# Kernel optimization log

Hardware: AMD Instinct MI355X
Metric: run time of the kernel (lower is better)

The kernel has to match this reference:

```python
import jax, jax.numpy as jnp
import numpy as np

B, P = 8, 1000          # batch_size, num_prots
N = B * P               # total PPI nodes
E = 512000              # edges (avg degree 64)
F_HPO = 1024            # HPO feature dim (num_features)
F_MOLP = 8192           # protein molecular feature dim (hardcoded)
F_MOLD = 1024           # drug molecular feature dim (hardcoded)
D = 200
EPS = 1e-8              # torch CosineSimilarity default eps


def leaky(x):
    return jax.nn.leaky_relu(x, 0.2)


def gcn_improved(x, W, b, src, dst):
    # PyG GCNConv(improved=True): A_hat = A + 2*I, symmetrically normalized.
    h = x @ W                                                   # [N,200]
    deg = jnp.zeros((x.shape[0],), x.dtype).at[dst].add(1.0) + 2.0
    dinv = jax.lax.rsqrt(deg)
    norm = dinv[src] * dinv[dst]                                # [E]
    out = jnp.zeros_like(h).at[dst].add(norm[:, None] * h[src])  # gather->scale->scatter
    out = out + (2.0 * dinv * dinv)[:, None] * h                # self loops with weight 2
    return out + b


def setup_inputs() -> dict:
    key = jax.random.key(0)
    ks = jax.random.split(key, 30)
    def W(i, shape):
        return jax.random.normal(ks[i], shape, jnp.float32) * (1.0 / float(np.sqrt(shape[0])))
    def bvec(i, n):
        return jax.random.normal(ks[i], (n,), jnp.float32) * 0.01
    return {
        # forward inputs
        'PPI_x': jax.random.normal(ks[0], (N, F_HPO), jnp.float32),
        'protein_mol_feature': jax.random.normal(ks[1], (N, F_MOLP), jnp.float32),
        'drug_feature': jax.random.normal(ks[2], (B, F_HPO), jnp.float32),
        'drug_mol_feature': jax.random.normal(ks[3], (B, F_MOLD), jnp.float32),
        'edge_index': jax.random.randint(ks[4], (2, E), 0, N, dtype=jnp.int32),
        # frozen HPO model heads (assumed Linear -> 200)
        'hpo_drug_W': W(5, (F_HPO, D)), 'hpo_drug_b': bvec(6, D),
        'hpo_prot_W': W(7, (F_HPO, D)), 'hpo_prot_b': bvec(8, D),
        # mol_protein_model: 8192 -> 256 -> 200
        'mp_W1': W(9, (F_MOLP, 256)), 'mp_b1': bvec(10, 256),
        'mp_W2': W(11, (256, D)), 'mp_b2': bvec(12, D),
        # mol_drug_model: 1024 -> 256 -> 200
        'md_W1': W(13, (F_MOLD, 256)), 'md_b1': bvec(14, 256),
        'md_W2': W(15, (256, D)), 'md_b2': bvec(16, D),
        # fusion linears
        'pl1_W': W(17, (2 * D, D)), 'pl1_b': bvec(18, D),
        'dl1_W': W(19, (2 * D, D)), 'dl1_b': bvec(20, D),
        'dl2_W': W(21, (D, D)), 'dl2_b': bvec(22, D),
        # GCN layers
        'g1_W': W(23, (D, D)), 'g1_b': bvec(24, D),
        'g2_W': W(25, (D, D)), 'g2_b': bvec(26, D),
    }


def reference(PPI_x, protein_mol_feature, drug_feature, drug_mol_feature, edge_index,
              hpo_drug_W, hpo_drug_b, hpo_prot_W, hpo_prot_b,
              mp_W1, mp_b1, mp_W2, mp_b2, md_W1, md_b1, md_W2, md_b2,
              pl1_W, pl1_b, dl1_W, dl1_b, dl2_W, dl2_b,
              g1_W, g1_b, g2_W, g2_b):
    src, dst = edge_index[0], edge_index[1]
    # protein branch (dropout is identity in eval)
    px = PPI_x @ hpo_prot_W + hpo_prot_b                                 # [N,200]
    pm = leaky(protein_mol_feature @ mp_W1 + mp_b1) @ mp_W2 + mp_b2      # [N,200]
    px = leaky(jnp.concatenate([px, pm], axis=1))                        # [N,400]
    px = px @ pl1_W + pl1_b                                              # [N,200]
    # drug branch
    df = drug_feature @ hpo_drug_W + hpo_drug_b                          # [B,200]
    dm = leaky(drug_mol_feature @ md_W1 + md_b1) @ md_W2 + md_b2         # [B,200]
    d = leaky(jnp.concatenate([dm, df], axis=1))                         # [B,400]
    d = leaky(d @ dl1_W + dl1_b)                                         # [B,200]
    d = d @ dl2_W + dl2_b                                                # [B,200]
    d = jnp.repeat(d, P, axis=0)                                         # [B*P,200]
    # two stacked GCN layers (no nonlinearity between, as in source)
    px = gcn_improved(px, g1_W, g1_b, src, dst)
    px = gcn_improved(px, g2_W, g2_b, src, dst)
    # per-row cosine similarity (torch.nn.CosineSimilarity(dim=1))
    num = jnp.sum(d * px, axis=1)
    den = jnp.maximum(jnp.linalg.norm(d, axis=1), EPS) * jnp.maximum(jnp.linalg.norm(px, axis=1), EPS)
    sim = num / den
    return jax.nn.sigmoid(sim.reshape(B, P))
```

## Files before the change

kernel.cpp:

```cpp
#include <hip/hip_runtime.h>
#include <cstdint>
#include <cstddef>

typedef uint16_t u16;
typedef __bf16 bf16x8 __attribute__((ext_vector_type(8)));
typedef short  s16x8  __attribute__((ext_vector_type(8)));
typedef float  f32x4  __attribute__((ext_vector_type(4)));

__device__ __forceinline__ u16 f2b(float f) {
    union { float f; uint32_t u; } v; v.f = f;
    uint32_t u = v.u;
    uint32_t r = (u + 0x7FFFu + ((u >> 16) & 1u)) >> 16;
    return (u16)r;
}
__device__ __forceinline__ float b2f(u16 h) {
    union { uint32_t u; float f; } v; v.u = ((uint32_t)h) << 16;
    return v.f;
}
__device__ __forceinline__ float leakyf(float x) { return x > 0.f ? x : 0.2f * x; }
__device__ __forceinline__ void unp4(uint2 u, float& f0, float& f1, float& f2, float& f3) {
    union { uint32_t u; float f; } t;
    t.u = u.x << 16;          f0 = t.f;
    t.u = u.x & 0xffff0000u;  f1 = t.f;
    t.u = u.y << 16;          f2 = t.f;
    t.u = u.y & 0xffff0000u;  f3 = t.f;
}

static constexpr int NN = 8000;
static constexpr int EE = 512000;
static constexpr int BB = 8;

#define GLOAD_LDS16(gp, lp)                                                              \
    __builtin_amdgcn_global_load_lds((const __attribute__((address_space(1))) void*)(gp), \
                                     (__attribute__((address_space(3))) void*)(lp), 16, 0, 0)

__global__ void conv_wT(const float* __restrict__ W, int Wn, int rows, int rowOff,
                        u16* __restrict__ Bt, int Kpad, int kOff, int kSpan) {
    __shared__ u16 tile[64][65];
    const int kb = blockIdx.x * 64, nb = blockIdx.y * 64;
    const int tid = threadIdx.x;
    const int ln = tid & 63, lw = tid >> 6;
    #pragma unroll
    for (int r = 0; r < 16; r++) {
        int kk = kb + lw * 16 + r;
        int n  = nb + ln;
        float v = (kk < rows && n < Wn) ? W[(size_t)(rowOff + kk) * Wn + n] : 0.f;
        tile[ln][lw * 16 + r] = f2b(v);
    }
    __syncthreads();
    #pragma unroll
    for (int r = 0; r < 16; r++) {
        int nl = lw * 16 + r;
        int kk = kb + ln;
        if (kk < kSpan) Bt[(size_t)(nb + nl) * Kpad + kOff + kk] = tile[nl][ln];
    }
}

__global__ void conv_wT5(const float* W_mp2, const float* W_pl1, const float* W_g1, const float* W_g2,
                         u16* Btmp2, u16* Btpl1, u16* Btg1, u16* Btg2) {
    __shared__ u16 tile[64][65];
    const float* W; int Wn, rows, rowOff; u16* Bt; int Kpad, kOff, kSpan;
    switch (blockIdx.z) {
        case 0: W = W_mp2; Wn = 200; rows = 256; rowOff = 0;   Bt = Btmp2; Kpad = 256; kOff = 0;   kSpan = 256; break;
        case 1: W = W_pl1; Wn = 200; rows = 200; rowOff = 0;   Bt = Btpl1; Kpad = 512; kOff = 0;   kSpan = 256; break;
        case 2: W = W_pl1; Wn = 200; rows = 200; rowOff = 200; Bt = Btpl1; Kpad = 512; kOff = 256; kSpan = 256; break;
        case 3: W = W_g1;  Wn = 200; rows = 200; rowOff = 0;   Bt = Btg1;  Kpad = 256; kOff = 0;   kSpan = 256; break;
        default:W = W_g2;  Wn = 200; rows = 200; rowOff = 0;   Bt = Btg2;  Kpad = 256; kOff = 0;   kSpan = 256; break;
    }
    const int kb = blockIdx.x * 64, nb = blockIdx.y * 64;
    const int tid = threadIdx.x;
    const int ln = tid & 63, lw = tid >> 6;
    #pragma unroll
    for (int r = 0; r < 16; r++) {
        int kk = kb + lw * 16 + r;
        int n  = nb + ln;
        float v = (kk < rows && n < Wn) ? W[(size_t)(rowOff + kk) * Wn + n] : 0.f;
        tile[ln][lw * 16 + r] = f2b(v);
    }
    __syncthreads();
    #pragma unroll
    for (int r = 0; r < 16; r++) {
        int nl = lw * 16 + r;
        int kk = kb + ln;
        if (kk < kSpan) Bt[(size_t)(nb + nl) * Kpad + kOff + kk] = tile[nl][ln];
    }
}

__global__ void padvec5(const float* p0, int n0, float* d0,
                        const float* p1, int n1, float* d1,
                        const float* p2, int n2, float* d2,
                        const float* p3, int n3, float* d3,
                        const float* p4, int n4, float* d4) {
    const float* p; int n; float* d;
    switch (blockIdx.x) {
        case 0: p = p0; n = n0; d = d0; break;
        case 1: p = p1; n = n1; d = d1; break;
        case 2: p = p2; n = n2; d = d2; break;
        case 3: p = p3; n = n3; d = d3; break;
        default: p = p4; n = n4; d = d4; break;
    }
    int i = threadIdx.x;
    d[i] = (p != nullptr && i < n) ? p[i] : 0.f;
}

__global__ void zero_i32(int* __restrict__ p, int n) {
    int i = blockIdx.x * 256 + threadIdx.x;
    if (i < n) p[i] = 0;
}

template<int BM>
__global__ __launch_bounds__(256) void gemm_kernel(
    const void* __restrict__ Ap, int a_is_f32, int lda,
    const u16* __restrict__ Bt, int K, int kLen,
    const float* __restrict__ bias,
    void* __restrict__ Cp, int cmode, int ldc, int do_leaky, size_t partStride) {
    constexpr int MREP = BM / 16;
    __shared__ u16 As[BM][72];
    __shared__ u16 Bs[16384];
    const int tid  = threadIdx.x;
    const int m0   = blockIdx.x * BM;
    const int kStart = blockIdx.y * kLen;
    const int wave = tid >> 6, lane = tid & 63;
    const int q = lane >> 4, r = lane & 15;
    const int wn = wave * 64;

    f32x4 acc[MREP][4];
    #pragma unroll
    for (int i = 0; i < MREP; i++)
        #pragma unroll
        for (int j = 0; j < 4; j++) acc[i][j] = (f32x4){0, 0, 0, 0};

    for (int k0 = kStart; k0 < kStart + kLen; k0 += 64) {
        #pragma unroll
        for (int c = 0; c < 8; ++c) {
            const int idx16 = c * 256 + tid;
            const int row   = idx16 >> 3;
            const int gs    = (idx16 & 7) ^ (row & 7);
            const u16* src  = Bt + (size_t)row * K + k0 + gs * 8;
            u16* dst = &Bs[0] + c * 2048 + wave * 512;
            GLOAD_LDS16(src, dst);
        }
        if (BM == 64) {
            const int ar = tid >> 2, ac = (tid & 3) * 16;
            if (a_is_f32) {
                const float* A = (const float*)Ap + (size_t)(m0 + ar) * lda + k0 + ac;
                float4 f0 = *(const float4*)(A + 0);
                float4 f1 = *(const float4*)(A + 4);
                float4 f2 = *(const float4*)(A + 8);
                float4 f3 = *(const float4*)(A + 12);
                u16 h[16];
                h[0]=f2b(f0.x); h[1]=f2b(f0.y); h[2]=f2b(f0.z); h[3]=f2b(f0.w);
                h[4]=f2b(f1.x); h[5]=f2b(f1.y); h[6]=f2b(f1.z); h[7]=f2b(f1.w);
                h[8]=f2b(f2.x); h[9]=f2b(f2.y); h[10]=f2b(f2.z); h[11]=f2b(f2.w);
                h[12]=f2b(f3.x); h[13]=f2b(f3.y); h[14]=f2b(f3.z); h[15]=f2b(f3.w);
                *(uint4*)(&As[ar][ac])     = ((uint4*)h)[0];
                *(uint4*)(&As[ar][ac + 8]) = ((uint4*)h)[1];
            } else {
                const u16* A = (const u16*)Ap + (size_t)(m0 + ar) * lda + k0 + ac;
                uint4 u0 = *(const uint4*)(A + 0);
                uint4 u1 = *(const uint4*)(A + 8);
                *(uint4*)(&As[ar][ac])     = u0;
                *(uint4*)(&As[ar][ac + 8]) = u1;
            }
        } else {
            const int ar = tid >> 3, ac = (tid & 7) * 8;
            if (a_is_f32) {
                const float* A = (const float*)Ap + (size_t)(m0 + ar) * lda + k0 + ac;
                float4 f0 = *(const float4*)(A + 0);
                float4 f1 = *(const float4*)(A + 4);
                u16 h[8];
                h[0]=f2b(f0.x); h[1]=f2b(f0.y); h[2]=f2b(f0.z); h[3]=f2b(f0.w);
                h[4]=f2b(f1.x); h[5]=f2b(f1.y); h[6]=f2b(f1.z); h[7]=f2b(f1.w);
                *(uint4*)(&As[ar][ac]) = *(uint4*)h;
            } else {
                const u16* A = (const u16*)Ap + (size_t)(m0 + ar) * lda + k0 + ac;
                *(uint4*)(&As[ar][ac]) = *(const uint4*)A;
            }
        }
        __syncthreads();
        #pragma unroll
        for (int ks = 0; ks < 2; ks++) {
            const int kb = ks * 32 + q * 8;
            s16x8 a[MREP];
            #pragma unroll
            for (int m = 0; m < MREP; m++) a[m] = *(const s16x8*)(&As[m * 16 + r][kb]);
            const int swz  = ((ks << 2) + q) ^ (r & 7);
            const int boff = ((wn + r) << 7) + (swz << 4);
            const char* BsC = (const char*)&Bs[0];
            s16x8 b[4];
            #pragma unroll
            for (int j = 0; j < 4; j++) b[j] = *(const s16x8*)(BsC + boff + j * 2048);
            #pragma unroll
            for (int m = 0; m < MREP; m++)
                #pragma unroll
                for (int j = 0; j < 4; j++)
                    acc[m][j] = __builtin_amdgcn_mfma_f32_16x16x32_bf16(
                        __builtin_bit_cast(bf16x8, a[m]), __builtin_bit_cast(bf16x8, b[j]),
                        acc[m][j], 0, 0, 0);
        }
        __syncthreads();
    }

    #pragma unroll
    for (int ti = 0; ti < MREP; ti++)
        #pragma unroll
        for (int tj = 0; tj < 4; tj++)
            #pragma unroll
            for (int reg = 0; reg < 4; reg++) {
                int gr = m0 + ti * 16 + q * 4 + reg;
                int gc = wn + tj * 16 + r;
                float v = acc[ti][tj][reg];
                if (cmode == 2) {
                    ((float*)Cp)[blockIdx.y * partStride + (size_t)gr * 256 + gc] = v;
                } else {
                    v += bias[gc];
                    if (do_leaky) v = leakyf(v);
                    if (cmode == 1) ((u16*)Cp)[(size_t)gr * ldc + gc] = f2b(v);
                    else            ((float*)Cp)[(size_t)gr * ldc + gc] = v;
                }
            }
}

__global__ void reduce_k(const float* __restrict__ part, size_t partStride, int S,
                         const float* __restrict__ bias, void* __restrict__ out,
                         int out_bf16, int ldc, int do_leaky) {
    int i = blockIdx.x * 256 + threadIdx.x;
    float v = 0.f;
    for (int s = 0; s < S; s++) v += part[s * partStride + i];
    int col = i & 255, row = i >> 8;
    v += bias[col];
    if (do_leaky) v = leakyf(v);
    if (out_bf16) ((u16*)out)[(size_t)row * ldc + col] = f2b(v);
    else          ((float*)out)[(size_t)row * ldc + col] = v;
}

__global__ void count_kernel(const int* __restrict__ dst, int* __restrict__ cnt) {
    int e = blockIdx.x * 256 + threadIdx.x;
    if (e < EE) atomicAdd(&cnt[dst[e]], 1);
}
__global__ void scan_kernel(const int* __restrict__ cnt, int* __restrict__ row_start,
                            int* __restrict__ cursor, float* __restrict__ dinv) {
    __shared__ int part[1024];
    const int tid = threadIdx.x;
    int local[8];
    int s = 0;
    const int base = tid * 8;
    #pragma unroll
    for (int j = 0; j < 8; j++) { int idx = base + j; int v = (idx < NN) ? cnt[idx] : 0; local[j] = s; s += v; }
    part[tid] = s;
    __syncthreads();
    for (int off = 1; off < 1024; off <<= 1) {
        int v = (tid >= off) ? part[tid - off] : 0;
        __syncthreads();
        part[tid] += v;
        __syncthreads();
    }
    const int excl = (tid == 0) ? 0 : part[tid - 1];
    #pragma unroll
    for (int j = 0; j < 8; j++) {
        int idx = base + j;
        if (idx < NN) {
            int v = excl + local[j];
            row_start[idx] = v; cursor[idx] = v;
            dinv[idx] = rsqrtf((float)cnt[idx] + 2.0f);
        }
    }
    if (tid == 1023) row_start[NN] = part[1023];
}
__global__ void fill_kernel(const int* __restrict__ src, const int* __restrict__ dst,
                            int* __restrict__ cursor, const float* __restrict__ dinv,
                            int* __restrict__ csr_src, float* __restrict__ csr_w) {
    int e = blockIdx.x * 256 + threadIdx.x;
    if (e < EE) {
        int s = src[e], d = dst[e];
        int pos = atomicAdd(&cursor[d], 1);
        csr_src[pos] = s;
        csr_w[pos]   = dinv[s] * dinv[d];
    }
}

__global__ __launch_bounds__(256) void agg_kernel(
    const u16* __restrict__ h, const float* __restrict__ dinv,
    const int* __restrict__ row_start, const int* __restrict__ csr_src,
    const float* __restrict__ csr_w, const float* __restrict__ bias,
    u16* __restrict__ out_bf16, const float* __restrict__ dhat,
    float* __restrict__ out_sig) {
    const int wave = threadIdx.x >> 6, lane = threadIdx.x & 63;
    const int node = blockIdx.x * 4 + wave;
    const int start = row_start[node], end = row_start[node + 1];
    const float di = dinv[node];

    float a0, a1, a2, a3;
    {
        uint2 hv = *(const uint2*)(h + (size_t)node * 256 + lane * 4);
        float f0, f1, f2, f3; unp4(hv, f0, f1, f2, f3);
        float sl = 2.f * di * di;
        a0 = sl * f0; a1 = sl * f1; a2 = sl * f2; a3 = sl * f3;
    }

    for (int p = start; p < end; p += 64) {
        const int n = min(64, end - p);
        int   mySrc = 0;
        float myW   = 0.f;
        if (lane < n) { mySrc = csr_src[p + lane]; myW = csr_w[p + lane]; }
        int j0 = 0;
        for (; j0 + 8 <= n; j0 += 8) {
            int sj[8]; float wj[8]; uint2 rj[8];
            #pragma unroll
            for (int j = 0; j < 8; j++) { sj[j] = __shfl(mySrc, j0 + j); wj[j] = __shfl(myW, j0 + j); }
            #pragma unroll
            for (int j = 0; j < 8; j++) rj[j] = *(const uint2*)(h + (size_t)sj[j] * 256 + lane * 4);
            #pragma unroll
            for (int j = 0; j < 8; j++) {
                float f0, f1, f2, f3; unp4(rj[j], f0, f1, f2, f3);
                a0 += wj[j] * f0; a1 += wj[j] * f1; a2 += wj[j] * f2; a3 += wj[j] * f3;
            }
        }
        for (; j0 < n; j0++) {
            int s = __shfl(mySrc, j0);
            float w = __shfl(myW, j0);
            uint2 rv = *(const uint2*)(h + (size_t)s * 256 + lane * 4);
            float f0, f1, f2, f3; unp4(rv, f0, f1, f2, f3);
            a0 += w * f0; a1 += w * f1; a2 += w * f2; a3 += w * f3;
        }
    }

    if (out_bf16 != nullptr) {
        uint2 o = {0u, 0u};
        if (lane < 50) {
            float4 bv = *(const float4*)(bias + lane * 4);
            u16 h0 = f2b(a0 + bv.x), h1 = f2b(a1 + bv.y), h2 = f2b(a2 + bv.z), h3 = f2b(a3 + bv.w);
            o.x = (uint32_t)h0 | ((uint32_t)h1 << 16);
            o.y = (uint32_t)h2 | ((uint32_t)h3 << 16);
        }
        *(uint2*)(out_bf16 + (size_t)node * 256 + lane * 4) = o;
    } else {
        float dot = 0.f, nn2 = 0.f;
        if (lane < 50) {
            float4 bv = *(const float4*)(bias + lane * 4);
            float4 dv = *(const float4*)(dhat + (node / 1000) * 200 + lane * 4);
            float v0 = a0 + bv.x, v1 = a1 + bv.y, v2 = a2 + bv.z, v3 = a3 + bv.w;
            dot = v0 * dv.x + v1 * dv.y + v2 * dv.z + v3 * dv.w;
            nn2 = v0 * v0 + v1 * v1 + v2 * v2 + v3 * v3;
        }
        #pragma unroll
        for (int off = 32; off; off >>= 1) {
            dot += __shfl_xor(dot, off, 64);
            nn2 += __shfl_xor(nn2, off, 64);
        }
        if (lane == 0) {
            float sim = dot / fmaxf(sqrtf(nn2), 1e-8f);
            out_sig[node] = 1.f / (1.f + expf(-sim));
        }
    }
}

__global__ void drug_kernel(const float* __restrict__ drugF, const float* __restrict__ drugM,
                            const float* __restrict__ hW, const float* __restrict__ hb,
                            const float* __restrict__ m1W, const float* __restrict__ m1b,
                            const float* __restrict__ m2W, const float* __restrict__ m2b,
                            const float* __restrict__ l1W, const float* __restrict__ l1b,
                            const float* __restrict__ l2W, const float* __restrict__ l2b,
                            float* __restrict__ dhat) {
    const int b = blockIdx.x, tid = threadIdx.x;
    __shared__ float sF[1024], sM[1024], sT[256], s400[400], s200[200], sred[256];
    for (int k = tid; k < 1024; k += 256) { sF[k] = drugF[b * 1024 + k]; sM[k] = drugM[b * 1024 + k]; }
    __syncthreads();
    {
        float acc = m1b[tid];
        for (int k = 0; k < 1024; k++) acc += sM[k] * m1W[k * 256 + tid];
        sT[tid] = leakyf(acc);
    }
    float dfv = 0.f;
    if (tid < 200) {
        dfv = hb[tid];
        for (int k = 0; k < 1024; k++) dfv += sF[k] * hW[k * 200 + tid];
    }
    __syncthreads();
    if (tid < 200) {
        float acc = m2b[tid];
        for (int k = 0; k < 256; k++) acc += sT[k] * m2W[k * 200 + tid];
        s400[tid]       = leakyf(acc);
        s400[200 + tid] = leakyf(dfv);
    }
    __syncthreads();
    if (tid < 200) {
        float acc = l1b[tid];
        for (int k = 0; k < 400; k++) acc += s400[k] * l1W[k * 200 + tid];
        s200[tid] = leakyf(acc);
    }
    __syncthreads();
    float dv = 0.f;
    if (tid < 200) {
        dv = l2b[tid];
        for (int k = 0; k < 200; k++) dv += s200[k] * l2W[k * 200 + tid];
    }
    sred[tid] = (tid < 200) ? dv * dv : 0.f;
    __syncthreads();
    for (int off = 128; off; off >>= 1) {
        if (tid < off) sred[tid] += sred[tid + off];
        __syncthreads();
    }
    float nrm = fmaxf(sqrtf(sred[0]), 1e-8f);
    if (tid < 200) dhat[b * 200 + tid] = dv / nrm;
}

extern "C" void kernel_launch(void* const* d_in, const int* in_sizes, int n_in,
                              void* d_out, int out_size, void* d_ws, size_t ws_size,
                              hipStream_t stream) {
    const float* PPI_x = (const float*)d_in[0];
    const float* PMF   = (const float*)d_in[1];
    const float* drugF = (const float*)d_in[2];
    const float* drugM = (const float*)d_in[3];
    const int*   eidx  = (const int*)d_in[4];
    const float* hpo_drug_W = (const float*)d_in[5];
    const float* hpo_drug_b = (const float*)d_in[6];
    const float* hpo_prot_W = (const float*)d_in[7];
    const float* hpo_prot_b = (const float*)d_in[8];
    const float* mp_W1 = (const float*)d_in[9];
    const float* mp_b1 = (const float*)d_in[10];
    const float* mp_W2 = (const float*)d_in[11];
    const float* mp_b2 = (const float*)d_in[12];
    const float* md_W1 = (const float*)d_in[13];
    const float* md_b1 = (const float*)d_in[14];
    const float* md_W2 = (const float*)d_in[15];
    const float* md_b2 = (const float*)d_in[16];
    const float* pl1_W = (const float*)d_in[17];
    const float* pl1_b = (const float*)d_in[18];
    const float* dl1_W = (const float*)d_in[19];
    const float* dl1_b = (const float*)d_in[20];
    const float* dl2_W = (const float*)d_in[21];
    const float* dl2_b = (const float*)d_in[22];
    const float* g1_W  = (const float*)d_in[23];
    const float* g1_b  = (const float*)d_in[24];
    const float* g2_W  = (const float*)d_in[25];
    const float* g2_b  = (const float*)d_in[26];

    char* wsp = (char*)d_ws;
    size_t off = 0;
    auto alloc = [&](size_t bytes) -> void* {
        size_t o = (off + 255) & ~(size_t)255;
        off = o + bytes;
        return (void*)(wsp + o);
    };

    u16* cb    = (u16*)alloc((size_t)NN * 512 * 2);
    u16* t1    = (u16*)alloc((size_t)NN * 256 * 2);
    u16* px2   = (u16*)alloc((size_t)NN * 256 * 2);
    u16* hbuf  = (u16*)alloc((size_t)NN * 256 * 2);
    float* part = (float*)alloc((size_t)4 * NN * 256 * 4);
    u16* Btmp1 = (u16*)alloc((size_t)256 * 8192 * 2);
    u16* Bthpo = (u16*)alloc((size_t)256 * 1024 * 2);
    u16* Btmp2 = (u16*)alloc((size_t)256 * 256 * 2);
    u16* Btpl1 = (u16*)alloc((size_t)256 * 512 * 2);
    u16* Btg1  = (u16*)alloc((size_t)256 * 256 * 2);
    u16* Btg2  = (u16*)alloc((size_t)256 * 256 * 2);
    float* bias_hpo = (float*)alloc(256 * 4);
    float* bias_m1  = (float*)alloc(256 * 4);
    float* bias_m2  = (float*)alloc(256 * 4);
    float* bias_pl  = (float*)alloc(256 * 4);
    float* zero256  = (float*)alloc(256 * 4);
    float* dhat     = (float*)alloc((size_t)BB * 200 * 4);
    int*   deg      = (int*)alloc((size_t)NN * 4);
    float* dinv     = (float*)alloc((size_t)NN * 4);
    int*   row_st   = (int*)alloc((size_t)(NN + 4) * 4);
    int*   cursor   = (int*)alloc((size_t)NN * 4);
    int*   csr_src  = (int*)alloc((size_t)EE * 4);
    float* csr_w    = (float*)alloc((size_t)EE * 4);

    u16* y1 = t1;
    const size_t PSTRIDE = (size_t)NN * 256;

    const int* e_src = eidx;
    const int* e_dst = eidx + EE;

    conv_wT<<<dim3(16, 4),  256, 0, stream>>>(hpo_prot_W, 200, 1024, 0, Bthpo, 1024, 0, 1024);
    conv_wT<<<dim3(128, 4), 256, 0, stream>>>(mp_W1,      256, 8192, 0, Btmp1, 8192, 0, 8192);
    conv_wT5<<<dim3(4, 4, 5), 256, 0, stream>>>(mp_W2, pl1_W, g1_W, g2_W, Btmp2, Btpl1, Btg1, Btg2);
    padvec5<<<5, 256, 0, stream>>>(hpo_prot_b, 200, bias_hpo,
                                   mp_b1,      256, bias_m1,
                                   mp_b2,      200, bias_m2,
                                   pl1_b,      200, bias_pl,
                                   nullptr,    0,   zero256);

    drug_kernel<<<BB, 256, 0, stream>>>(drugF, drugM, hpo_drug_W, hpo_drug_b,
                                        md_W1, md_b1, md_W2, md_b2,
                                        dl1_W, dl1_b, dl2_W, dl2_b, dhat);

    const int RG = (NN * 256) / 256;

    gemm_kernel<64><<<dim3(125, 4), 256, 0, stream>>>(PPI_x, 1, 1024, Bthpo, 1024, 256, zero256, part, 2, 256, 0, PSTRIDE);
    reduce_k<<<RG, 256, 0, stream>>>(part, PSTRIDE, 4, bias_hpo, cb, 1, 512, 1);
    gemm_kernel<64><<<dim3(125, 4), 256, 0, stream>>>(PMF, 1, 8192, Btmp1, 8192, 2048, zero256, part, 2, 256, 0, PSTRIDE);
    reduce_k<<<RG, 256, 0, stream>>>(part, PSTRIDE, 4, bias_m1, t1, 1, 256, 1);
    gemm_kernel<32><<<dim3(250, 1), 256, 0, stream>>>(t1, 0, 256, Btmp2, 256, 256, bias_m2, cb + 256, 1, 512, 1, 0);
    gemm_kernel<32><<<dim3(250, 1), 256, 0, stream>>>(cb, 0, 512, Btpl1, 512, 512, bias_pl, px2, 1, 256, 0, 0);

    zero_i32<<<(NN + 255) / 256, 256, 0, stream>>>(deg, NN);
    count_kernel<<<EE / 256, 256, 0, stream>>>(e_dst, deg);
    scan_kernel<<<1, 1024, 0, stream>>>(deg, row_st, cursor, dinv);
    fill_kernel<<<EE / 256, 256, 0, stream>>>(e_src, e_dst, cursor, dinv, csr_src, csr_w);

    gemm_kernel<32><<<dim3(250, 1), 256, 0, stream>>>(px2, 0, 256, Btg1, 256, 256, zero256, hbuf, 1, 256, 0, 0);
    agg_kernel<<<NN / 4, 256, 0, stream>>>(hbuf, dinv, row_st, csr_src, csr_w, g1_b, y1, nullptr, nullptr);
    gemm_kernel<32><<<dim3(250, 1), 256, 0, stream>>>(y1, 0, 256, Btg2, 256, 256, zero256, hbuf, 1, 256, 0, 0);
    agg_kernel<<<NN / 4, 256, 0, stream>>>(hbuf, dinv, row_st, csr_src, csr_w, g2_b, nullptr, dhat, (float*)d_out);
}
```

Baseline: 822.5 us.

## Merge split-K reductions, double PMF split-K, fold degree zeroing into prep kernel

The PMF GEMM split-K factor goes from 4 to 8 (kLen 1024), and the HPO GEMM writes its partials into a separate region of a larger partial buffer. One reduce kernel then sums both sets of partials and applies bias and leaky for t1 and cb, replacing two reduce launches. Degree-array zeroing is folded into the bias padding kernel, removing a launch. The larger split-K raises partial-buffer traffic (12 fp32 slabs of N×256) in exchange for more parallelism in the dominant 8192-K GEMM.

Measured after the change: 835.6 us. About the same (+1.6%).

```diff
diff --git a/kernel.cpp b/kernel.cpp
--- a/kernel.cpp
+++ b/kernel.cpp
@@ -86,26 +86,26 @@
     }
 }
 
-__global__ void padvec5(const float* p0, int n0, float* d0,
-                        const float* p1, int n1, float* d1,
-                        const float* p2, int n2, float* d2,
-                        const float* p3, int n3, float* d3,
-                        const float* p4, int n4, float* d4) {
-    const float* p; int n; float* d;
-    switch (blockIdx.x) {
-        case 0: p = p0; n = n0; d = d0; break;
-        case 1: p = p1; n = n1; d = d1; break;
-        case 2: p = p2; n = n2; d = d2; break;
-        case 3: p = p3; n = n3; d = d3; break;
-        default: p = p4; n = n4; d = d4; break;
-    }
-    int i = threadIdx.x;
-    d[i] = (p != nullptr && i < n) ? p[i] : 0.f;
-}
-
-__global__ void zero_i32(int* __restrict__ p, int n) {
-    int i = blockIdx.x * 256 + threadIdx.x;
-    if (i < n) p[i] = 0;
+__global__ void prep_kernel(const float* p0, int n0, float* d0,
+                            const float* p1, int n1, float* d1,
+                            const float* p2, int n2, float* d2,
+                            const float* p3, int n3, float* d3,
+                            const float* p4, int n4, float* d4,
+                            int* __restrict__ deg) {
+    const int bx = blockIdx.x, tid = threadIdx.x;
+    if (bx < 5) {
+        const float* p; int n; float* d;
+        switch (bx) {
+            case 0: p = p0; n = n0; d = d0; break;
+            case 1: p = p1; n = n1; d = d1; break;
+            case 2: p = p2; n = n2; d = d2; break;
+            case 3: p = p3; n = n3; d = d3; break;
+            default: p = p4; n = n4; d = d4; break;
+        }
+        d[tid] = (p != nullptr && tid < n) ? p[tid] : 0.f;
+    }
+    const int base = bx * 250;
+    if (tid < 250) deg[base + tid] = 0;
 }
 
 template<int BM>
@@ -221,17 +221,19 @@
             }
 }
 
-__global__ void reduce_k(const float* __restrict__ part, size_t partStride, int S,
-                         const float* __restrict__ bias, void* __restrict__ out,
-                         int out_bf16, int ldc, int do_leaky) {
+__global__ void reduce2(const float* __restrict__ part, size_t PS,
+                        const float* __restrict__ bias_m1, u16* __restrict__ t1,
+                        const float* __restrict__ bias_hpo, u16* __restrict__ cb) {
     int i = blockIdx.x * 256 + threadIdx.x;
+    int col = i & 255, row = i >> 8;
     float v = 0.f;
-    for (int s = 0; s < S; s++) v += part[s * partStride + i];
-    int col = i & 255, row = i >> 8;
-    v += bias[col];
-    if (do_leaky) v = leakyf(v);
-    if (out_bf16) ((u16*)out)[(size_t)row * ldc + col] = f2b(v);
-    else          ((float*)out)[(size_t)row * ldc + col] = v;
+    #pragma unroll
+    for (int s = 0; s < 8; s++) v += part[(size_t)s * PS + i];
+    t1[(size_t)row * 256 + col] = f2b(leakyf(v + bias_m1[col]));
+    float w = 0.f;
+    #pragma unroll
+    for (int s = 8; s < 12; s++) w += part[(size_t)s * PS + i];
+    cb[(size_t)row * 512 + col] = f2b(leakyf(w + bias_hpo[col]));
 }
 
 __global__ void count_kernel(const int* __restrict__ dst, int* __restrict__ cnt) {
@@ -448,7 +450,7 @@
     u16* t1    = (u16*)alloc((size_t)NN * 256 * 2);
     u16* px2   = (u16*)alloc((size_t)NN * 256 * 2);
     u16* hbuf  = (u16*)alloc((size_t)NN * 256 * 2);
-    float* part = (float*)alloc((size_t)4 * NN * 256 * 4);
+    float* part = (float*)alloc((size_t)12 * NN * 256 * 4);
     u16* Btmp1 = (u16*)alloc((size_t)256 * 8192 * 2);
     u16* Bthpo = (u16*)alloc((size_t)256 * 1024 * 2);
     u16* Btmp2 = (u16*)alloc((size_t)256 * 256 * 2);
@@ -477,11 +479,11 @@
     conv_wT<<<dim3(16, 4),  256, 0, stream>>>(hpo_prot_W, 200, 1024, 0, Bthpo, 1024, 0, 1024);
     conv_wT<<<dim3(128, 4), 256, 0, stream>>>(mp_W1,      256, 8192, 0, Btmp1, 8192, 0, 8192);
     conv_wT5<<<dim3(4, 4, 5), 256, 0, stream>>>(mp_W2, pl1_W, g1_W, g2_W, Btmp2, Btpl1, Btg1, Btg2);
-    padvec5<<<5, 256, 0, stream>>>(hpo_prot_b, 200, bias_hpo,
-                                   mp_b1,      256, bias_m1,
-                                   mp_b2,      200, bias_m2,
-                                   pl1_b,      200, bias_pl,
-                                   nullptr,    0,   zero256);
+    prep_kernel<<<32, 256, 0, stream>>>(hpo_prot_b, 200, bias_hpo,
+                                        mp_b1,      256, bias_m1,
+                                        mp_b2,      200, bias_m2,
+                                        pl1_b,      200, bias_pl,
+                                        nullptr,    0,   zero256, deg);
 
     drug_kernel<<<BB, 256, 0, stream>>>(drugF, drugM, hpo_drug_W, hpo_drug_b,
                                         md_W1, md_b1, md_W2, md_b2,
@@ -489,14 +491,14 @@
 
     const int RG = (NN * 256) / 256;
 
-    gemm_kernel<64><<<dim3(125, 4), 256, 0, stream>>>(PPI_x, 1, 1024, Bthpo, 1024, 256, zero256, part, 2, 256, 0, PSTRIDE);
-    reduce_k<<<RG, 256, 0, stream>>>(part, PSTRIDE, 4, bias_hpo, cb, 1, 512, 1);
-    gemm_kernel<64><<<dim3(125, 4), 256, 0, stream>>>(PMF, 1, 8192, Btmp1, 8192, 2048, zero256, part, 2, 256, 0, PSTRIDE);
-    reduce_k<<<RG, 256, 0, stream>>>(part, PSTRIDE, 4, bias_m1, t1, 1, 256, 1);
+    gemm_kernel<64><<<dim3(125, 4), 256, 0, stream>>>(PPI_x, 1, 1024, Bthpo, 1024, 256, zero256,
+                                                      part + 8 * PSTRIDE, 2, 256, 0, PSTRIDE);
+    gemm_kernel<64><<<dim3(125, 8), 256, 0, stream>>>(PMF, 1, 8192, Btmp1, 8192, 1024, zero256,
+                                                      part, 2, 256, 0, PSTRIDE);
+    reduce2<<<RG, 256, 0, stream>>>(part, PSTRIDE, bias_m1, t1, bias_hpo, cb);
     gemm_kernel<32><<<dim3(250, 1), 256, 0, stream>>>(t1, 0, 256, Btmp2, 256, 256, bias_m2, cb + 256, 1, 512, 1, 0);
     gemm_kernel<32><<<dim3(250, 1), 256, 0, stream>>>(cb, 0, 512, Btpl1, 512, 512, bias_pl, px2, 1, 256, 0, 0);
 
-    zero_i32<<<(NN + 255) / 256, 256, 0, stream>>>(deg, NN);
     count_kernel<<<EE / 256, 256, 0, stream>>>(e_dst, deg);
     scan_kernel<<<1, 1024, 0, stream>>>(deg, row_st, cursor, dinv);
     fill_kernel<<<EE / 256, 256, 0, stream>>>(e_src, e_dst, cursor, dinv, csr_src, csr_w);
```
